# Performance work log

Hardware: AMD Instinct MI355X
Metric: run time of the kernel (lower is better)

## Reference

```python
import jax, jax.numpy as jnp
import numpy as np

K = 16            # neighbors
RATIO = 0.25      # sampling ratio -> M = N*RATIO
EPS = 1e-5        # BatchNorm eps


def _fps(pts, m):
    # Farthest point sampling for one cloud. pts: (N,3) -> (m,) int32 indices.
    n = pts.shape[0]

    def body(carry, _):
        dist, last = carry                      # dist: (N,) min sq-dist to selected set
        d = jnp.sum((pts - pts[last]) ** 2, axis=-1)
        dist = jnp.minimum(dist, d)
        nxt = jnp.argmax(dist).astype(jnp.int32)
        return (dist, nxt), nxt

    init = (jnp.full((n,), jnp.inf, pts.dtype), jnp.int32(0))
    _, rest = jax.lax.scan(body, init, None, length=m - 1)
    return jnp.concatenate([jnp.zeros((1,), jnp.int32), rest])


def setup_inputs() -> dict:
    key = jax.random.key(0)
    ks = jax.random.split(key, 3)
    B, N, C_IN, C_OUT = 8, 8192, 64, 128
    x = jax.random.normal(ks[0], (B, N, C_IN), jnp.float32)
    p = jax.random.normal(ks[1], (B, N, 3), jnp.float32)
    W = jax.random.normal(ks[2], (C_OUT, C_IN), jnp.float32) * 0.05
    gamma = jnp.ones((C_OUT,), jnp.float32)
    beta = jnp.zeros((C_OUT,), jnp.float32)
    run_mean = jnp.zeros((C_OUT,), jnp.float32)
    run_var = jnp.ones((C_OUT,), jnp.float32)
    return {"x": x, "p": p, "W": W, "gamma": gamma, "beta": beta,
            "run_mean": run_mean, "run_var": run_var}


def reference(x, p, W, gamma, beta, run_mean, run_var):
    B, N, _ = x.shape
    M = int(N * RATIO)

    # 1) FPS sample M points per cloud
    idx_fps = jax.vmap(lambda q: _fps(q, M))(p)                   # (B, M)
    p_out = jnp.take_along_axis(p, idx_fps[..., None], axis=1)    # (B, M, 3)

    # 2) KNN: squared distances (B, M, N), sorted K nearest via top_k on -dist
    d2 = (jnp.sum(p_out ** 2, -1)[..., None]
          + jnp.sum(p ** 2, -1)[:, None, :]
          - 2.0 * jnp.einsum('bmd,bnd->bmn', p_out, p))
    _, nbr = jax.lax.top_k(-d2, K)                                # (B, M, K) ascending dist

    # 3) Pointwise MLP: Conv1d(k=1, no bias) == matmul, then BN (eval) + ReLU
    h = jnp.einsum('bnc,oc->bno', x, W)                           # (B, N, C_OUT)
    h = (h - run_mean) * jax.lax.rsqrt(run_var + EPS) * gamma + beta
    h = jax.nn.relu(h)

    # 4) Gather neighbor features and max-pool over K
    flat = nbr.reshape(B, M * K)
    feats = jnp.take_along_axis(h, flat[..., None], axis=1).reshape(B, M, K, -1)
    y = jnp.max(feats, axis=2)                                    # (B, M, C_OUT)
    return y, p_out
```

## Files before the change

kernel.cpp:

```cpp
#include <hip/hip_runtime.h>

#define B_   8
#define N_   8192
#define CIN  64
#define COUT 128
#define M_   2048
#define K_   16

template <int CTRL>
__device__ __forceinline__ unsigned long long dpp64(unsigned long long x) {
  int lo = (int)(unsigned)(x & 0xFFFFFFFFull);
  int hi = (int)(unsigned)(x >> 32);
  int dlo = __builtin_amdgcn_update_dpp(lo, lo, CTRL, 0xF, 0xF, false);
  int dhi = __builtin_amdgcn_update_dpp(hi, hi, CTRL, 0xF, 0xF, false);
  return ((unsigned long long)(unsigned)dhi << 32) | (unsigned)dlo;
}

__device__ __forceinline__ unsigned long long readlane63_u64(unsigned long long k) {
  unsigned lo = (unsigned)__builtin_amdgcn_readlane((int)(unsigned)(k & 0xFFFFFFFFull), 63);
  unsigned hi = (unsigned)__builtin_amdgcn_readlane((int)(unsigned)(k >> 32), 63);
  return ((unsigned long long)hi << 32) | lo;
}

__device__ __forceinline__ unsigned long long wave_max_u64(unsigned long long k) {
  unsigned long long t;
  t = dpp64<0x111>(k); k = t > k ? t : k;
  t = dpp64<0x112>(k); k = t > k ? t : k;
  t = dpp64<0x114>(k); k = t > k ? t : k;
  t = dpp64<0x118>(k); k = t > k ? t : k;
  t = dpp64<0x142>(k); k = t > k ? t : k;
  t = dpp64<0x143>(k); k = t > k ? t : k;
  return readlane63_u64(k);
}

__device__ __forceinline__ unsigned long long wave_min_u64(unsigned long long k) {
  unsigned long long t;
  t = dpp64<0x111>(k); k = t < k ? t : k;
  t = dpp64<0x112>(k); k = t < k ? t : k;
  t = dpp64<0x114>(k); k = t < k ? t : k;
  t = dpp64<0x118>(k); k = t < k ? t : k;
  t = dpp64<0x142>(k); k = t < k ? t : k;
  t = dpp64<0x143>(k); k = t < k ? t : k;
  return readlane63_u64(k);
}

#define MROWS 16

__global__ __launch_bounds__(256) void mlp_kernel(
    const float* __restrict__ x, const float* __restrict__ W,
    const float* __restrict__ gamma, const float* __restrict__ beta,
    const float* __restrict__ rmean, const float* __restrict__ rvar,
    float* __restrict__ h) {
  __shared__ float wt[CIN * 132];
  __shared__ float xs[MROWS * CIN];

  const int t  = threadIdx.x;
  const int o  = t & 127;
  const int rg = t >> 7;
  const int rowBase = blockIdx.x * MROWS;

  for (int idx = t; idx < COUT * CIN; idx += 256) {
    const int oo = idx >> 6, cc = idx & 63;
    wt[cc * 132 + oo] = W[idx];
  }
  ((float4*)xs)[t] = ((const float4*)(x + (size_t)rowBase * CIN))[t];
  __syncthreads();

  float acc[8] = {0.f, 0.f, 0.f, 0.f, 0.f, 0.f, 0.f, 0.f};
#pragma unroll
  for (int c4 = 0; c4 < CIN / 4; c4++) {
    const float w0 = wt[(4 * c4 + 0) * 132 + o];
    const float w1 = wt[(4 * c4 + 1) * 132 + o];
    const float w2 = wt[(4 * c4 + 2) * 132 + o];
    const float w3 = wt[(4 * c4 + 3) * 132 + o];
#pragma unroll
    for (int i = 0; i < 8; i++) {
      const float4 xv = *(const float4*)&xs[(rg * 8 + i) * CIN + c4 * 4];
      acc[i] += xv.x * w0 + xv.y * w1 + xv.z * w2 + xv.w * w3;
    }
  }

  const float mu = rmean[o];
  const float sc = rsqrtf(rvar[o] + 1e-5f) * gamma[o];
  const float bt = beta[o];
#pragma unroll
  for (int i = 0; i < 8; i++) {
    const float v = (acc[i] - mu) * sc + bt;
    h[(size_t)(rowBase + rg * 8 + i) * COUT + o] = fmaxf(v, 0.f);
  }
}

#define FTH 512
#define FPT 16

__global__ __launch_bounds__(512) void fps_kernel(
    const float* __restrict__ p, float* __restrict__ p_out) {
#pragma clang fp contract(off)
  __shared__ float4 pc4[N_];
  __shared__ __align__(16) unsigned long long wred[2][8];
  __shared__ int idxHist[M_];

  const int b   = blockIdx.x;
  const int tid = threadIdx.x;
  const int wv  = tid >> 6;
  const int ln  = tid & 63;

  const float* pb = p + (size_t)b * N_ * 3;
  for (int n = tid; n < N_; n += FTH)
    pc4[n] = make_float4(pb[3 * n + 0], pb[3 * n + 1], pb[3 * n + 2], 0.f);
  if (tid == 0) idxHist[0] = 0;
  __syncthreads();

  float4 c0 = pc4[0];
  float cx = c0.x, cy = c0.y, cz = c0.z;

  float X[FPT], Y[FPT], Z[FPT], D[FPT];
#pragma unroll
  for (int k = 0; k < FPT; k++) {
    float4 v = pc4[tid + k * FTH];
    X[k] = v.x; Y[k] = v.y; Z[k] = v.z;
    D[k] = __builtin_inff();
  }

  int buf = 0;
  for (int it = 1; it < M_; ++it) {
    float bd = -1.0f; int bk = 0;
#pragma unroll
    for (int k = 0; k < FPT; k++) {
      float dx = X[k] - cx, dy = Y[k] - cy, dz = Z[k] - cz;
      float d  = (dx * dx + dy * dy) + dz * dz;
      float dm = fminf(D[k], d);
      D[k] = dm;
      if (dm > bd) { bd = dm; bk = k; }
    }
    const int n = tid + (bk << 9);
    unsigned long long key =
        ((unsigned long long)__float_as_uint(bd) << 32) |
        (unsigned)(N_ - 1 - n);
    key = wave_max_u64(key);
    if (ln == 0) wred[buf][wv] = key;
    __syncthreads();
    const ulonglong2* wp = (const ulonglong2*)(&wred[buf][0]);
    ulonglong2 w0 = wp[0], w1 = wp[1], w2 = wp[2], w3 = wp[3];
    unsigned long long m0 = w0.x > w0.y ? w0.x : w0.y;
    unsigned long long m1 = w1.x > w1.y ? w1.x : w1.y;
    unsigned long long m2 = w2.x > w2.y ? w2.x : w2.y;
    unsigned long long m3 = w3.x > w3.y ? w3.x : w3.y;
    m0 = m0 > m1 ? m0 : m1;
    m2 = m2 > m3 ? m2 : m3;
    m0 = m0 > m2 ? m0 : m2;
    const int nw = N_ - 1 - (int)(unsigned)(m0 & 0xFFFFFFFFu);
    float4 cc = pc4[nw];
    cx = cc.x; cy = cc.y; cz = cc.z;
    if (tid == 0) idxHist[it] = nw;
    buf ^= 1;
  }
  __syncthreads();

  float* po = p_out + (size_t)b * M_ * 3;
  for (int mi = tid; mi < M_; mi += FTH) {
    float4 v = pc4[idxHist[mi]];
    po[mi * 3 + 0] = v.x;
    po[mi * 3 + 1] = v.y;
    po[mi * 3 + 2] = v.z;
  }
}

#define UMAXK 0xFFFFFFFFFFFFFFFFull
#define QPB  16

__global__ __launch_bounds__(1024) void knn_kernel(
    const float* __restrict__ p, const float* __restrict__ p_out,
    const float* __restrict__ h, float* __restrict__ y) {
#pragma clang fp contract(off)
  __shared__ float4 pc4[N_];
  __shared__ int winLds[QPB][K_];

  const int t    = threadIdx.x;
  const int wv   = t >> 6;
  const int lane = t & 63;
  const int b    = blockIdx.x & 7;
  const int grp  = blockIdx.x >> 3;
  const int q    = b * M_ + grp * QPB + wv;

  const float* pb = p + (size_t)b * N_ * 3;
  for (int n = t; n < N_; n += 1024) {
    float xx = pb[3 * n + 0], yy = pb[3 * n + 1], zz = pb[3 * n + 2];
    float sn = (xx * xx + yy * yy) + zz * zz;
    pc4[n] = make_float4(xx, yy, zz, sn);
  }
  __syncthreads();

  const float qx = p_out[q * 3 + 0];
  const float qy = p_out[q * 3 + 1];
  const float qz = p_out[q * 3 + 2];
  const float sq = (qx * qx + qy * qy) + qz * qz;

  unsigned long long c0 = UMAXK, c1 = UMAXK, c2 = UMAXK, c3 = UMAXK;
#pragma unroll 4
  for (int j = 0; j < 128; j++) {
    const int n = lane + (j << 6);
    float4 v = pc4[n];
    float dot = __builtin_fmaf(qz, v.z,
                __builtin_fmaf(qy, v.y, qx * v.x));
    float d2 = (sq + v.w) - 2.0f * dot;
    unsigned u = __float_as_uint(d2);
    u ^= (unsigned)((int)u >> 31) | 0x80000000u;
    unsigned long long key = ((unsigned long long)u << 32) | (unsigned)n;
    if (key < c3) {
      unsigned long long x = key, mn;
      mn = x < c0 ? x : c0; x = x < c0 ? c0 : x; c0 = mn;
      mn = x < c1 ? x : c1; x = x < c1 ? c1 : x; c1 = mn;
      mn = x < c2 ? x : c2; x = x < c2 ? c2 : x; c2 = mn;
      c3 = x < c3 ? x : c3;
    }
  }

  int count = 4;
  unsigned long long em0 = 0ull, em1 = 0ull;
  unsigned long long mykey = UMAXK;

  for (int k = 0; k < K_; k++) {
    unsigned long long cnd = (count > 0) ? c0 : UMAXK;
    unsigned long long win = wave_min_u64(cnd);
    if (lane == k) mykey = win;
    const int nstar = (int)(unsigned)(win & 0xFFFFFFFFu);
    if ((nstar & 63) == lane) {
      const int j = nstar >> 6;
      if (j < 64) em0 |= 1ull << j; else em1 |= 1ull << (j - 64);
      c0 = c1; c1 = c2; c2 = c3; c3 = UMAXK; count--;
      if (count == 0 && k < K_ - 1) {
        c0 = c1 = c2 = c3 = UMAXK;
        for (int j2 = 0; j2 < 128; j2++) {
          bool ex = (j2 < 64) ? ((em0 >> j2) & 1ull) : ((em1 >> (j2 - 64)) & 1ull);
          if (!ex) {
            const int n2 = lane + (j2 << 6);
            float4 v = pc4[n2];
            float dot = __builtin_fmaf(qz, v.z,
                        __builtin_fmaf(qy, v.y, qx * v.x));
            float d2 = (sq + v.w) - 2.0f * dot;
            unsigned u = __float_as_uint(d2);
            u ^= (unsigned)((int)u >> 31) | 0x80000000u;
            unsigned long long kk = ((unsigned long long)u << 32) | (unsigned)n2;
            if (kk < c3) {
              unsigned long long x = kk, mn;
              mn = x < c0 ? x : c0; x = x < c0 ? c0 : x; c0 = mn;
              mn = x < c1 ? x : c1; x = x < c1 ? c1 : x; c1 = mn;
              mn = x < c2 ? x : c2; x = x < c2 ? c2 : x; c2 = mn;
              c3 = x < c3 ? x : c3;
            }
          }
        }
        count = 4;
      }
    }
  }

  if (lane < K_) winLds[wv][lane] = (int)(unsigned)(mykey & 0xFFFFFFFFu);
  __syncthreads();

  const float* hb = h + (size_t)b * N_ * COUT;
  float2 acc = make_float2(-__builtin_inff(), -__builtin_inff());
#pragma unroll
  for (int i = 0; i < K_; i++) {
    const int n = winLds[wv][i];
    float2 v = *(const float2*)(hb + (size_t)n * COUT + lane * 2);
    acc.x = fmaxf(acc.x, v.x);
    acc.y = fmaxf(acc.y, v.y);
  }
  *(float2*)(y + (size_t)q * COUT + lane * 2) = acc;
}

extern "C" void kernel_launch(void* const* d_in, const int* in_sizes, int n_in,
                              void* d_out, int out_size, void* d_ws, size_t ws_size,
                              hipStream_t stream) {
  const float* x     = (const float*)d_in[0];
  const float* p     = (const float*)d_in[1];
  const float* W     = (const float*)d_in[2];
  const float* gamma = (const float*)d_in[3];
  const float* beta  = (const float*)d_in[4];
  const float* rmean = (const float*)d_in[5];
  const float* rvar  = (const float*)d_in[6];

  float* y     = (float*)d_out;
  float* p_out = y + (size_t)B_ * M_ * COUT;
  float* h     = (float*)d_ws;

  mlp_kernel<<<(B_ * N_) / MROWS, 256, 0, stream>>>(
      x, W, gamma, beta, rmean, rvar, h);
  fps_kernel<<<B_, FTH, 0, stream>>>(p, p_out);
  knn_kernel<<<B_ * (M_ / QPB), 1024, 0, stream>>>(p, p_out, h, y);
}
```

Baseline: 2.285 ms.

## Fuse MLP into FPS launch, pack FPS math as float2, DPP cross-wave reduce

Merges the MLP and FPS kernels into one launch. The first 8 blocks run farthest point sampling while the remaining blocks compute the pointwise MLP, so the serial FPS loop can overlap with the MLP work. The FPS distance math now uses 2-wide float vectors, which allows packed FP32 instructions. The cross-wave max now uses DPP shuffles instead of each thread reading all 8 LDS slots. The shared-memory footprint of about 137KB per block now applies to the MLP blocks too, which limits their occupancy to one block per CU. The scheduling order of the FPS blocks relative to the MLP blocks is also not guaranteed.

```diff
diff --git a/kernel.cpp b/kernel.cpp
--- a/kernel.cpp
+++ b/kernel.cpp
@@ -6,6 +6,8 @@
 #define COUT 128
 #define M_   2048
 #define K_   16
+
+typedef float v2f __attribute__((ext_vector_type(2)));
 
 template <int CTRL>
 __device__ __forceinline__ unsigned long long dpp64(unsigned long long x) {
@@ -16,9 +18,9 @@
   return ((unsigned long long)(unsigned)dhi << 32) | (unsigned)dlo;
 }
 
-__device__ __forceinline__ unsigned long long readlane63_u64(unsigned long long k) {
-  unsigned lo = (unsigned)__builtin_amdgcn_readlane((int)(unsigned)(k & 0xFFFFFFFFull), 63);
-  unsigned hi = (unsigned)__builtin_amdgcn_readlane((int)(unsigned)(k >> 32), 63);
+__device__ __forceinline__ unsigned long long readlane_u64(unsigned long long k, int l) {
+  unsigned lo = (unsigned)__builtin_amdgcn_readlane((int)(unsigned)(k & 0xFFFFFFFFull), l);
+  unsigned hi = (unsigned)__builtin_amdgcn_readlane((int)(unsigned)(k >> 32), l);
   return ((unsigned long long)hi << 32) | lo;
 }
 
@@ -30,7 +32,7 @@
   t = dpp64<0x118>(k); k = t > k ? t : k;
   t = dpp64<0x142>(k); k = t > k ? t : k;
   t = dpp64<0x143>(k); k = t > k ? t : k;
-  return readlane63_u64(k);
+  return readlane_u64(k, 63);
 }
 
 __device__ __forceinline__ unsigned long long wave_min_u64(unsigned long long k) {
@@ -41,69 +43,71 @@
   t = dpp64<0x118>(k); k = t < k ? t : k;
   t = dpp64<0x142>(k); k = t < k ? t : k;
   t = dpp64<0x143>(k); k = t < k ? t : k;
-  return readlane63_u64(k);
-}
-
-#define MROWS 16
-
-__global__ __launch_bounds__(256) void mlp_kernel(
+  return readlane_u64(k, 63);
+}
+
+#define FTH 512
+#define FPT 16
+#define MROWS2 32
+
+__global__ __launch_bounds__(512) void fps_mlp_kernel(
+    const float* __restrict__ p, float* __restrict__ p_out,
     const float* __restrict__ x, const float* __restrict__ W,
     const float* __restrict__ gamma, const float* __restrict__ beta,
     const float* __restrict__ rmean, const float* __restrict__ rvar,
     float* __restrict__ h) {
-  __shared__ float wt[CIN * 132];
-  __shared__ float xs[MROWS * CIN];
-
-  const int t  = threadIdx.x;
-  const int o  = t & 127;
-  const int rg = t >> 7;
-  const int rowBase = blockIdx.x * MROWS;
-
-  for (int idx = t; idx < COUT * CIN; idx += 256) {
-    const int oo = idx >> 6, cc = idx & 63;
-    wt[cc * 132 + oo] = W[idx];
-  }
-  ((float4*)xs)[t] = ((const float4*)(x + (size_t)rowBase * CIN))[t];
-  __syncthreads();
-
-  float acc[8] = {0.f, 0.f, 0.f, 0.f, 0.f, 0.f, 0.f, 0.f};
-#pragma unroll
-  for (int c4 = 0; c4 < CIN / 4; c4++) {
-    const float w0 = wt[(4 * c4 + 0) * 132 + o];
-    const float w1 = wt[(4 * c4 + 1) * 132 + o];
-    const float w2 = wt[(4 * c4 + 2) * 132 + o];
-    const float w3 = wt[(4 * c4 + 3) * 132 + o];
+#pragma clang fp contract(off)
+  __shared__ __align__(16) unsigned char smem[139776];
+
+  const int tid = threadIdx.x;
+
+  if (blockIdx.x >= 8) {
+    float* wt = (float*)smem;
+    float* xs = (float*)(smem + 33792);
+
+    const int o  = tid & 127;
+    const int rg = tid >> 7;
+    const int rowBase = (blockIdx.x - 8) * MROWS2;
+
+    for (int idx = tid; idx < COUT * CIN; idx += 512) {
+      const int oo = idx >> 6, cc = idx & 63;
+      wt[cc * 132 + oo] = W[idx];
+    }
+    ((float4*)xs)[tid] = ((const float4*)(x + (size_t)rowBase * CIN))[tid];
+    __syncthreads();
+
+    float acc[8] = {0.f, 0.f, 0.f, 0.f, 0.f, 0.f, 0.f, 0.f};
+#pragma unroll
+    for (int c4 = 0; c4 < CIN / 4; c4++) {
+      const float w0 = wt[(4 * c4 + 0) * 132 + o];
+      const float w1 = wt[(4 * c4 + 1) * 132 + o];
+      const float w2 = wt[(4 * c4 + 2) * 132 + o];
+      const float w3 = wt[(4 * c4 + 3) * 132 + o];
+#pragma unroll
+      for (int i = 0; i < 8; i++) {
+        const float4 xv = *(const float4*)&xs[(rg * 8 + i) * CIN + c4 * 4];
+        acc[i] += xv.x * w0 + xv.y * w1 + xv.z * w2 + xv.w * w3;
+      }
+    }
+    const float mu = rmean[o];
+    const float sc = rsqrtf(rvar[o] + 1e-5f) * gamma[o];
+    const float bt = beta[o];
 #pragma unroll
     for (int i = 0; i < 8; i++) {
-      const float4 xv = *(const float4*)&xs[(rg * 8 + i) * CIN + c4 * 4];
-      acc[i] += xv.x * w0 + xv.y * w1 + xv.z * w2 + xv.w * w3;
-    }
-  }
-
-  const float mu = rmean[o];
-  const float sc = rsqrtf(rvar[o] + 1e-5f) * gamma[o];
-  const float bt = beta[o];
-#pragma unroll
-  for (int i = 0; i < 8; i++) {
-    const float v = (acc[i] - mu) * sc + bt;
-    h[(size_t)(rowBase + rg * 8 + i) * COUT + o] = fmaxf(v, 0.f);
-  }
-}
-
-#define FTH 512
-#define FPT 16
-
-__global__ __launch_bounds__(512) void fps_kernel(
-    const float* __restrict__ p, float* __restrict__ p_out) {
-#pragma clang fp contract(off)
-  __shared__ float4 pc4[N_];
-  __shared__ __align__(16) unsigned long long wred[2][8];
-  __shared__ int idxHist[M_];
-
-  const int b   = blockIdx.x;
-  const int tid = threadIdx.x;
-  const int wv  = tid >> 6;
-  const int ln  = tid & 63;
+      const float v = (acc[i] - mu) * sc + bt;
+      h[(size_t)(rowBase + rg * 8 + i) * COUT + o] = fmaxf(v, 0.f);
+    }
+    return;
+  }
+
+  float4* pc4 = (float4*)smem;
+  unsigned long long (*wred)[8] =
+      (unsigned long long (*)[8])(smem + 131072);
+  int* idxHist = (int*)(smem + 131072 + 128);
+
+  const int b  = blockIdx.x;
+  const int wv = tid >> 6;
+  const int ln = tid & 63;
 
   const float* pb = p + (size_t)b * N_ * 3;
   for (int n = tid; n < N_; n += FTH)
@@ -114,24 +118,35 @@
   float4 c0 = pc4[0];
   float cx = c0.x, cy = c0.y, cz = c0.z;
 
-  float X[FPT], Y[FPT], Z[FPT], D[FPT];
-#pragma unroll
-  for (int k = 0; k < FPT; k++) {
-    float4 v = pc4[tid + k * FTH];
-    X[k] = v.x; Y[k] = v.y; Z[k] = v.z;
-    D[k] = __builtin_inff();
+  v2f X2[8], Y2[8], Z2[8], D2[8];
+#pragma unroll
+  for (int j = 0; j < 8; j++) {
+    float4 a = pc4[tid + (2 * j) * FTH];
+    float4 c = pc4[tid + (2 * j + 1) * FTH];
+    X2[j] = (v2f){a.x, c.x};
+    Y2[j] = (v2f){a.y, c.y};
+    Z2[j] = (v2f){a.z, c.z};
+    D2[j] = (v2f){__builtin_inff(), __builtin_inff()};
   }
 
   int buf = 0;
   for (int it = 1; it < M_; ++it) {
+    const v2f cxv = {cx, cx}, cyv = {cy, cy}, czv = {cz, cz};
     float bd = -1.0f; int bk = 0;
 #pragma unroll
-    for (int k = 0; k < FPT; k++) {
-      float dx = X[k] - cx, dy = Y[k] - cy, dz = Z[k] - cz;
-      float d  = (dx * dx + dy * dy) + dz * dz;
-      float dm = fminf(D[k], d);
-      D[k] = dm;
-      if (dm > bd) { bd = dm; bk = k; }
+    for (int j = 0; j < 8; j++) {
+      v2f dx = X2[j] - cxv;
+      v2f dy = Y2[j] - cyv;
+      v2f dz = Z2[j] - czv;
+      v2f m1 = dx * dx;
+      v2f m2 = dy * dy;
+      v2f s  = m1 + m2;
+      v2f m3 = dz * dz;
+      v2f d  = s + m3;
+      v2f dm = __builtin_elementwise_min(D2[j], d);
+      D2[j] = dm;
+      if (dm.x > bd) { bd = dm.x; bk = 2 * j; }
+      if (dm.y > bd) { bd = dm.y; bk = 2 * j + 1; }
     }
     const int n = tid + (bk << 9);
     unsigned long long key =
@@ -140,16 +155,13 @@
     key = wave_max_u64(key);
     if (ln == 0) wred[buf][wv] = key;
     __syncthreads();
-    const ulonglong2* wp = (const ulonglong2*)(&wred[buf][0]);
-    ulonglong2 w0 = wp[0], w1 = wp[1], w2 = wp[2], w3 = wp[3];
-    unsigned long long m0 = w0.x > w0.y ? w0.x : w0.y;
-    unsigned long long m1 = w1.x > w1.y ? w1.x : w1.y;
-    unsigned long long m2 = w2.x > w2.y ? w2.x : w2.y;
-    unsigned long long m3 = w3.x > w3.y ? w3.x : w3.y;
-    m0 = m0 > m1 ? m0 : m1;
-    m2 = m2 > m3 ? m2 : m3;
-    m0 = m0 > m2 ? m0 : m2;
-    const int nw = N_ - 1 - (int)(unsigned)(m0 & 0xFFFFFFFFu);
+    unsigned long long kk = wred[buf][ln & 7];
+    unsigned long long t;
+    t = dpp64<0x111>(kk); kk = t > kk ? t : kk;
+    t = dpp64<0x112>(kk); kk = t > kk ? t : kk;
+    t = dpp64<0x114>(kk); kk = t > kk ? t : kk;
+    const unsigned long long m = readlane_u64(kk, 7);
+    const int nw = N_ - 1 - (int)(unsigned)(m & 0xFFFFFFFFu);
     float4 cc = pc4[nw];
     cx = cc.x; cy = cc.y; cz = cc.z;
     if (tid == 0) idxHist[it] = nw;
@@ -208,11 +220,11 @@
     u ^= (unsigned)((int)u >> 31) | 0x80000000u;
     unsigned long long key = ((unsigned long long)u << 32) | (unsigned)n;
     if (key < c3) {
-      unsigned long long x = key, mn;
-      mn = x < c0 ? x : c0; x = x < c0 ? c0 : x; c0 = mn;
-      mn = x < c1 ? x : c1; x = x < c1 ? c1 : x; c1 = mn;
-      mn = x < c2 ? x : c2; x = x < c2 ? c2 : x; c2 = mn;
-      c3 = x < c3 ? x : c3;
+      unsigned long long x2 = key, mn;
+      mn = x2 < c0 ? x2 : c0; x2 = x2 < c0 ? c0 : x2; c0 = mn;
+      mn = x2 < c1 ? x2 : c1; x2 = x2 < c1 ? c1 : x2; c1 = mn;
+      mn = x2 < c2 ? x2 : c2; x2 = x2 < c2 ? c2 : x2; c2 = mn;
+      c3 = x2 < c3 ? x2 : c3;
     }
   }
 
@@ -241,13 +253,13 @@
             float d2 = (sq + v.w) - 2.0f * dot;
             unsigned u = __float_as_uint(d2);
             u ^= (unsigned)((int)u >> 31) | 0x80000000u;
-            unsigned long long kk = ((unsigned long long)u << 32) | (unsigned)n2;
-            if (kk < c3) {
-              unsigned long long x = kk, mn;
-              mn = x < c0 ? x : c0; x = x < c0 ? c0 : x; c0 = mn;
-              mn = x < c1 ? x : c1; x = x < c1 ? c1 : x; c1 = mn;
-              mn = x < c2 ? x : c2; x = x < c2 ? c2 : x; c2 = mn;
-              c3 = x < c3 ? x : c3;
+            unsigned long long kk2 = ((unsigned long long)u << 32) | (unsigned)n2;
+            if (kk2 < c3) {
+              unsigned long long x2 = kk2, mn;
+              mn = x2 < c0 ? x2 : c0; x2 = x2 < c0 ? c0 : x2; c0 = mn;
+              mn = x2 < c1 ? x2 : c1; x2 = x2 < c1 ? c1 : x2; c1 = mn;
+              mn = x2 < c2 ? x2 : c2; x2 = x2 < c2 ? c2 : x2; c2 = mn;
+              c3 = x2 < c3 ? x2 : c3;
             }
           }
         }
@@ -286,8 +298,7 @@
   float* p_out = y + (size_t)B_ * M_ * COUT;
   float* h     = (float*)d_ws;
 
-  mlp_kernel<<<(B_ * N_) / MROWS, 256, 0, stream>>>(
-      x, W, gamma, beta, rmean, rvar, h);
-  fps_kernel<<<B_, FTH, 0, stream>>>(p, p_out);
+  fps_mlp_kernel<<<8 + (B_ * N_) / MROWS2, 512, 0, stream>>>(
+      p, p_out, x, W, gamma, beta, rmean, rvar, h);
   knn_kernel<<<B_ * (M_ / QPB), 1024, 0, stream>>>(p, p_out, h, y);
 }
```

Result: faster. 2.117 ms (-7.3%).
